# Kernel tuning notes

Measured on AMD Instinct MI355X. Metric: run time of the kernel, lower is better.

The kernel has to match this reference:

```python
import jax, jax.numpy as jnp
import numpy as np
from jax import lax


def setup_inputs() -> dict:
    key = jax.random.key(0)
    ks = jax.random.split(key, 4)
    B, Cin, H, W = 8, 64, 128, 128
    Cout, kh, kw = 64, 3, 3
    K = kh * kw
    x = jax.random.normal(ks[0], (B, Cin, H, W), jnp.float32)
    # small init so predicted offsets stay in a sensible range
    w_offset = jax.random.normal(ks[1], (2 * K, Cin, kh, kw), jnp.float32) * 0.01
    b_offset = jnp.zeros((2 * K,), jnp.float32)
    w_conv = jax.random.normal(ks[2], (Cout, Cin, kh, kw), jnp.float32) * (1.0 / np.sqrt(Cin * K))
    b_conv = jax.random.normal(ks[3], (Cout,), jnp.float32) * 0.01
    return dict(x=x, w_offset=w_offset, b_offset=b_offset, w_conv=w_conv, b_conv=b_conv)


def _deform_conv2d(x, offset, w, b, stride=(1, 1), padding=(1, 1), dilation=(1, 1)):
    B, Cin, Hin, Win = x.shape
    Cout, _, kh, kw = w.shape
    K = kh * kw
    sh, sw = stride; ph, pw = padding; dh, dw = dilation
    Hout = (Hin + 2 * ph - dh * (kh - 1) - 1) // sh + 1
    Wout = (Win + 2 * pw - dw * (kw - 1) - 1) // sw + 1
    # torchvision layout: [B, K, (dy,dx), Hout, Wout]
    off = offset.reshape(B, K, 2, Hout, Wout)
    dy, dx = off[:, :, 0], off[:, :, 1]
    hs = jnp.arange(Hout, dtype=x.dtype) * sh - ph          # [Hout]
    ws = jnp.arange(Wout, dtype=x.dtype) * sw - pw          # [Wout]
    ky = jnp.repeat(jnp.arange(kh, dtype=x.dtype) * dh, kw)  # [K]
    kx = jnp.tile(jnp.arange(kw, dtype=x.dtype) * dw, kh)    # [K]
    py = dy + (ky[:, None, None] + hs[None, :, None])[None]  # [B,K,Hout,Wout]
    px = dx + (kx[:, None, None] + ws[None, None, :])[None]

    def sample(img, py, px):
        y0 = jnp.floor(py); x0 = jnp.floor(px)
        wy1 = py - y0; wx1 = px - x0
        wy0 = 1.0 - wy1; wx0 = 1.0 - wx1

        def gather(yy, xx, wgt):
            valid = (yy >= 0) & (yy <= Hin - 1) & (xx >= 0) & (xx <= Win - 1)
            yi = jnp.clip(yy, 0, Hin - 1).astype(jnp.int32)
            xi = jnp.clip(xx, 0, Win - 1).astype(jnp.int32)
            vals = img[:, yi, xi]  # [Cin,K,Hout,Wout]
            return vals * (wgt * valid)[None]

        return (gather(y0, x0, wy0 * wx0) + gather(y0, x0 + 1, wy0 * wx1)
                + gather(y0 + 1, x0, wy1 * wx0) + gather(y0 + 1, x0 + 1, wy1 * wx1))

    sampled = jax.vmap(sample)(x, py, px)  # [B,Cin,K,Hout,Wout]
    out = jnp.einsum('bckhw,ock->bohw', sampled, w.reshape(Cout, Cin, K))
    return out + b[None, :, None, None]


def reference(x, w_offset, b_offset, w_conv, b_conv):
    # offset-predicting conv (stride 1, same padding, dilation 1)
    offset = lax.conv_general_dilated(
        x, w_offset, window_strides=(1, 1), padding=[(1, 1), (1, 1)],
        rhs_dilation=(1, 1), dimension_numbers=('NCHW', 'OIHW', 'NCHW'))
    offset = offset + b_offset[None, :, None, None]
    # deformable conv v1 (mask is None in _get_deformation)
    return _deform_conv2d(x, offset, w_conv, b_conv)
```

## Files before the change

### kernel.cpp

```cpp
#include <hip/hip_runtime.h>
#include <stdint.h>

#define H 128
#define W 128
#define CIN 64
#define COUT 64
#define NB 8
#define WR 4
#define WC 16
#define CW 20
#define NR 8
#define PLANE 162
#define REDS 260

typedef __attribute__((ext_vector_type(4))) float f32x4;
typedef __attribute__((ext_vector_type(2))) _Float16 f16x2;
typedef __attribute__((ext_vector_type(8))) _Float16 f16x8;
typedef __attribute__((ext_vector_type(4))) unsigned int u32x4;
typedef __attribute__((ext_vector_type(2))) unsigned int u32x2;

__device__ __forceinline__ f16x2 bch2(unsigned u) { return __builtin_bit_cast(f16x2, u); }
__device__ __forceinline__ unsigned bcu(f16x2 v) { return __builtin_bit_cast(unsigned, v); }

__global__ __launch_bounds__(256) void x_to_nhwc(const float* __restrict__ x,
                                                 _Float16* __restrict__ xt) {
    __shared__ _Float16 tile[W][68];
    int bh = blockIdx.x;
    int h = bh & (H - 1), b = bh >> 7;
    int t = threadIdx.x;
    #pragma unroll
    for (int i = 0; i < 8; ++i) {
        int idx = i * 256 + t;
        int c = idx >> 5;
        int w4 = (idx & 31) << 2;
        f32x4 v = *(const f32x4*)(x + (((size_t)(b * CIN + c) * H + h) * W + w4));
        #pragma unroll
        for (int j = 0; j < 4; ++j) tile[w4 + j][c] = (_Float16)v[j];
    }
    __syncthreads();
    _Float16* dst = xt + (size_t)bh * W * CIN;
    #pragma unroll
    for (int i = 0; i < 8; ++i) {
        int idx = i * 256 + t;
        int w = idx >> 4;
        int c4 = (idx & 15) << 2;
        *(uint2*)(dst + (size_t)w * CIN + c4) = *(const uint2*)&tile[w][c4];
    }
}

__global__ __launch_bounds__(256) void prep_w(const float* __restrict__ wo,
                                              const float* __restrict__ wc,
                                              _Float16* __restrict__ wao2,
                                              _Float16* __restrict__ wac2) {
    int t = blockIdx.x * 256 + threadIdx.x;
    if (t < 18432) {
        int j = t & 7, l = (t >> 3) & 63, m = (t >> 9) & 1, kk = t >> 10;
        int cout = m * 16 + (l & 15);
        int cin = (kk & 1) * 32 + ((l >> 4) << 3) + j;
        wao2[t] = (cout < 18) ? (_Float16)wo[(cout * 64 + cin) * 9 + (kk >> 1)]
                              : (_Float16)0.f;
    } else if (t < 18432 + 36864) {
        int u = t - 18432;
        int j = u & 7, l = (u >> 3) & 63, m = (u >> 9) & 3, kk = u >> 11;
        int cout = m * 16 + (l & 15);
        int cin = (kk & 1) * 32 + ((l >> 4) << 3) + j;
        wac2[u] = (_Float16)wc[(cout * 64 + cin) * 9 + (kk >> 1)];
    }
}

__global__ __launch_bounds__(256, 4) void deform_fused(const _Float16* __restrict__ xt,
                                                       const _Float16* __restrict__ wao2,
                                                       const _Float16* __restrict__ wac2,
                                                       const float* __restrict__ bo,
                                                       const float* __restrict__ bconv,
                                                       float* __restrict__ out) {
    __shared__ u32x4 s_x[8 * PLANE];
    __shared__ float s_meta[4][432];

    int bid = blockIdx.x;
    int b = bid & 7;
    int r = bid >> 3;
    int h0 = ((r >> 3) & 31) << 2;
    int w0 = (r & 7) << 4;
    int vy = h0 - 2, vx = w0 - 2;

    int t = threadIdx.x;
    int lane = t & 63, wv = t >> 6;
    int q = wv & 1;
    int half = wv >> 1;
    int pcol = lane & 15, hq = lane >> 4;
    int pl = half * 4 + hq;
    int r0 = h0 + 2 * q, r1 = r0 + 1;
    int wp = w0 + pcol;

    const _Float16* xb = xt + (size_t)b * H * W * CIN;

    for (int i = t; i < NR * CW * 8; i += 256) {
        int ch = i & 7;
        int q2 = i >> 3;
        int rr = q2 / CW;
        int cs = q2 - rr * CW;
        int row = min(max(vy + rr, 0), H - 1);
        int col = min(max(vx + cs, 0), W - 1);
        s_x[ch * PLANE + rr * CW + cs] =
            *(const u32x4*)(xb + (size_t)(row * W + col) * CIN + (ch << 3));
    }
    __syncthreads();

    const u32x4* sp = s_x + pl * PLANE;

    f32x4 aA0 = {}, aA1 = {}, aB0 = {}, aB1 = {};
    #pragma unroll
    for (int k = 0; k < 9; ++k) {
        int ky = k / 3 - 1, kx = k % 3 - 1;
        int xx = wp + kx;
        bool vx_ok = (unsigned)xx < (unsigned)W;
        int xc = min(max(xx, 0), W - 1) - vx;
        int yyA = r0 + ky, yyB = r1 + ky;
        int sA = (min(max(yyA, 0), H - 1) - vy) * CW + xc;
        int sB = (min(max(yyB, 0), H - 1) - vy) * CW + xc;
        u32x4 vA = sp[sA], vB = sp[sB];
        u32x4 z = {};
        if (!(vx_ok && (unsigned)yyA < (unsigned)H)) vA = z;
        if (!(vx_ok && (unsigned)yyB < (unsigned)H)) vB = z;
        f16x8 bfA = __builtin_bit_cast(f16x8, vA);
        f16x8 bfB = __builtin_bit_cast(f16x8, vB);
        const _Float16* wb = wao2 + (size_t)(4 * k + 2 * half) * 512 + lane * 8;
        f16x8 a0 = *(const f16x8*)(wb);
        f16x8 a1 = *(const f16x8*)(wb + 512);
        aA0 = __builtin_amdgcn_mfma_f32_16x16x32_f16(a0, bfA, aA0, 0, 0, 0);
        aA1 = __builtin_amdgcn_mfma_f32_16x16x32_f16(a1, bfA, aA1, 0, 0, 0);
        aB0 = __builtin_amdgcn_mfma_f32_16x16x32_f16(a0, bfB, aB0, 0, 0, 0);
        aB1 = __builtin_amdgcn_mfma_f32_16x16x32_f16(a1, bfB, aB1, 0, 0, 0);
    }

    if (half == 1) {
        float* scA = s_meta[2 * q] + lane * 6;
        scA[0] = aA0[0]; scA[1] = aA0[1]; scA[2] = aA0[2]; scA[3] = aA0[3];
        scA[4] = aA1[0]; scA[5] = aA1[1];
        float* scB = s_meta[2 * q + 1] + lane * 6;
        scB[0] = aB0[0]; scB[1] = aB0[1]; scB[2] = aB0[2]; scB[3] = aB0[3];
        scB[4] = aB1[0]; scB[5] = aB1[1];
    }
    __syncthreads();

    if (half == 0) {
        const float* scA = s_meta[2 * q] + lane * 6;
        const float* scB = s_meta[2 * q + 1] + lane * 6;
        float pA[6], pB[6];
        #pragma unroll
        for (int i = 0; i < 6; ++i) { pA[i] = scA[i]; pB[i] = scB[i]; }
        aA0[0] += pA[0]; aA0[1] += pA[1]; aA0[2] += pA[2]; aA0[3] += pA[3];
        aA1[0] += pA[4]; aA1[1] += pA[5];
        aB0[0] += pB[0]; aB0[1] += pB[1]; aB0[2] += pB[2]; aB0[3] += pB[3];
        aB1[0] += pB[4]; aB1[1] += pB[5];

        auto setup = [&](float* mrow, int row, int k, float dy, float dx) {
            float py = (float)(row + k / 3 - 1) + dy;
            float px = (float)(wp + k % 3 - 1) + dx;
            float y0f = floorf(py), x0f = floorf(px);
            float fy = py - y0f, fx = px - x0f;
            float vy0 = (y0f >= 0.f  && y0f <= 127.f) ? 1.f : 0.f;
            float vy1 = (y0f >= -1.f && y0f <= 126.f) ? 1.f : 0.f;
            float vx0 = (x0f >= 0.f  && x0f <= 127.f) ? 1.f : 0.f;
            float vx1 = (x0f >= -1.f && x0f <= 126.f) ? 1.f : 0.f;
            float g0 = (1.f - fy) * (1.f - fx) * vy0 * vx0;
            float g1 = (1.f - fy) * fx         * vy0 * vx1;
            float g2 = fy * (1.f - fx)         * vy1 * vx0;
            float g3 = fy * fx                 * vy1 * vx1;
            int y0i = (int)fminf(fmaxf(y0f, 0.f), 127.f);
            int x0i = (int)fminf(fmaxf(x0f, 0.f), 127.f);
            int y1i = (int)fminf(fmaxf(y0f + 1.f, 0.f), 127.f);
            int x1i = (int)fminf(fmaxf(x0f + 1.f, 0.f), 127.f);
            unsigned dxb = (unsigned)(x1i - x0i);
            unsigned dyb = (unsigned)(y1i - y0i);
            bool inw = (y0i >= vy) && (y1i <= vy + NR - 1) &&
                       (x0i >= vx) && (x1i <= vx + CW - 1);
            unsigned s00 = inw ? (unsigned)((y0i - vy) * CW + (x0i - vx)) : 0u;
            unsigned a00 = (unsigned)(y0i * W + x0i);
            unsigned awv = s00 | (dxb << 9) | (dyb << 10) | (inw ? 0u : (1u << 11)) | (a00 << 12);
            int idx = k * 16 + pcol;
            ((unsigned*)mrow)[idx] = awv;
            ((unsigned*)mrow)[144 + 2 * idx]     = bcu((f16x2){(_Float16)g0, (_Float16)g1});
            ((unsigned*)mrow)[144 + 2 * idx + 1] = bcu((f16x2){(_Float16)g2, (_Float16)g3});
        };
        f32x4 bo4 = *(const f32x4*)(bo + 4 * hq);
        setup(s_meta[2 * q],     r0, 2 * hq,     aA0[0] + bo4[0], aA0[1] + bo4[1]);
        setup(s_meta[2 * q],     r0, 2 * hq + 1, aA0[2] + bo4[2], aA0[3] + bo4[3]);
        setup(s_meta[2 * q + 1], r1, 2 * hq,     aB0[0] + bo4[0], aB0[1] + bo4[1]);
        setup(s_meta[2 * q + 1], r1, 2 * hq + 1, aB0[2] + bo4[2], aB0[3] + bo4[3]);
        if (hq == 0) {
            setup(s_meta[2 * q],     r0, 8, aA1[0] + bo[16], aA1[1] + bo[17]);
            setup(s_meta[2 * q + 1], r1, 8, aB1[0] + bo[16], aB1[1] + bo[17]);
        }
    }
    __syncthreads();

    const _Float16* xh = xb + (pl << 3);
    const unsigned* mA = (const unsigned*)s_meta[2 * q];
    const unsigned* mB = (const unsigned*)s_meta[2 * q + 1];
    f32x4 accA[4] = {}, accB[4] = {};

    #pragma unroll
    for (int k = 0; k < 9; ++k) {
        int idx = k * 16 + pcol;
        unsigned awA = mA[idx];
        unsigned awB = mB[idx];
        u32x2 wqA = *(const u32x2*)&mA[144 + 2 * idx];
        u32x2 wqB = *(const u32x2*)&mB[144 + 2 * idx];
        unsigned sA = awA & 511u, dxA = (awA >> 9) & 1u, dyA = (awA >> 10) & 1u;
        unsigned sB = awB & 511u, dxB = (awB >> 9) & 1u, dyB = (awB >> 10) & 1u;
        u32x4 a00 = sp[sA], a01 = sp[sA + dxA];
        u32x4 a10 = sp[sA + dyA * CW], a11 = sp[sA + dyA * CW + dxA];
        u32x4 b00 = sp[sB], b01 = sp[sB + dxB];
        u32x4 b10 = sp[sB + dyB * CW], b11 = sp[sB + dyB * CW + dxB];
        if (__builtin_expect((awA & (1u << 11)) != 0u, 0)) {
            unsigned a0_ = awA >> 12;
            a00 = *(const u32x4*)(xh + (size_t)a0_ * CIN);
            a01 = *(const u32x4*)(xh + (size_t)(a0_ + dxA) * CIN);
            a10 = *(const u32x4*)(xh + (size_t)(a0_ + (dyA << 7)) * CIN);
            a11 = *(const u32x4*)(xh + (size_t)(a0_ + (dyA << 7) + dxA) * CIN);
        }
        if (__builtin_expect((awB & (1u << 11)) != 0u, 0)) {
            unsigned b0_ = awB >> 12;
            b00 = *(const u32x4*)(xh + (size_t)b0_ * CIN);
            b01 = *(const u32x4*)(xh + (size_t)(b0_ + dxB) * CIN);
            b10 = *(const u32x4*)(xh + (size_t)(b0_ + (dyB << 7)) * CIN);
            b11 = *(const u32x4*)(xh + (size_t)(b0_ + (dyB << 7) + dxB) * CIN);
        }
        f16x2 wa = bch2(wqA[0]), wc_ = bch2(wqA[1]);
        f16x2 A00 = (f16x2){wa[0], wa[0]},  A01 = (f16x2){wa[1], wa[1]};
        f16x2 A10 = (f16x2){wc_[0], wc_[0]}, A11 = (f16x2){wc_[1], wc_[1]};
        f16x2 wb_ = bch2(wqB[0]), wd_ = bch2(wqB[1]);
        f16x2 B00 = (f16x2){wb_[0], wb_[0]}, B01 = (f16x2){wb_[1], wb_[1]};
        f16x2 B10 = (f16x2){wd_[0], wd_[0]}, B11 = (f16x2){wd_[1], wd_[1]};
        u32x4 frA, frB;
        #pragma unroll
        for (int d = 0; d < 4; ++d) {
            f16x2 vA = bch2(a00[d]) * A00 + bch2(a01[d]) * A01
                     + bch2(a10[d]) * A10 + bch2(a11[d]) * A11;
            f16x2 vB = bch2(b00[d]) * B00 + bch2(b01[d]) * B01
                     + bch2(b10[d]) * B10 + bch2(b11[d]) * B11;
            frA[d] = bcu(vA);
            frB[d] = bcu(vB);
        }
        f16x8 bfA = __builtin_bit_cast(f16x8, frA);
        f16x8 bfB = __builtin_bit_cast(f16x8, frB);
        const _Float16* ab = wac2 + (size_t)(8 * k + 4 * half) * 512 + lane * 8;
        #pragma unroll
        for (int m = 0; m < 4; ++m) {
            f16x8 wm = *(const f16x8*)(ab + m * 512);
            accA[m] = __builtin_amdgcn_mfma_f32_16x16x32_f16(wm, bfA, accA[m], 0, 0, 0);
            accB[m] = __builtin_amdgcn_mfma_f32_16x16x32_f16(wm, bfB, accB[m], 0, 0, 0);
        }
    }

    __syncthreads();
    float* red = (float*)s_x;
    if (half == 0) {
        #pragma unroll
        for (int m = 0; m < 4; ++m)
            #pragma unroll
            for (int r2 = 0; r2 < 4; ++r2)
                red[(m * 4 + r2) * REDS + q * 64 + lane] = accA[m][r2];
    }
    __syncthreads();
    if (half == 1) {
        #pragma unroll
        for (int m = 0; m < 4; ++m) {
            f32x4 bc4 = *(const f32x4*)(bconv + m * 16 + (hq << 2));
            #pragma unroll
            for (int r2 = 0; r2 < 4; ++r2) {
                int co = (m << 4) + (hq << 2) + r2;
                float v = accA[m][r2] + red[(m * 4 + r2) * REDS + q * 64 + lane] + bc4[r2];
                out[(((size_t)b * COUT + co) * H + r0) * W + wp] = v;
            }
        }
    }
    __syncthreads();
    if (half == 0) {
        #pragma unroll
        for (int m = 0; m < 4; ++m)
            #pragma unroll
            for (int r2 = 0; r2 < 4; ++r2)
                red[(m * 4 + r2) * REDS + q * 64 + lane] = accB[m][r2];
    }
    __syncthreads();
    if (half == 1) {
        #pragma unroll
        for (int m = 0; m < 4; ++m) {
            f32x4 bc4 = *(const f32x4*)(bconv + m * 16 + (hq << 2));
            #pragma unroll
            for (int r2 = 0; r2 < 4; ++r2) {
                int co = (m << 4) + (hq << 2) + r2;
                float v = accB[m][r2] + red[(m * 4 + r2) * REDS + q * 64 + lane] + bc4[r2];
                out[(((size_t)b * COUT + co) * H + r1) * W + wp] = v;
            }
        }
    }
}

extern "C" void kernel_launch(void* const* d_in, const int* in_sizes, int n_in,
                              void* d_out, int out_size, void* d_ws, size_t ws_size,
                              hipStream_t stream) {
    const float* x  = (const float*)d_in[0];
    const float* wo = (const float*)d_in[1];
    const float* bo = (const float*)d_in[2];
    const float* wc = (const float*)d_in[3];
    const float* bc = (const float*)d_in[4];
    float* out = (float*)d_out;

    _Float16* xt   = (_Float16*)d_ws;
    _Float16* wao2 = (_Float16*)((char*)d_ws + (size_t)NB * H * W * CIN * 2);
    _Float16* wac2 = wao2 + 18432;

    x_to_nhwc<<<NB * H, 256, 0, stream>>>(x, xt);
    prep_w<<<(18432 + 36864 + 255) / 256, 256, 0, stream>>>(wo, wc, wao2, wac2);
    deform_fused<<<NB * H * W / (WR * WC), 256, 0, stream>>>(xt, wao2, wac2, bo, bc, out);
}
```

Measured before the change: 49.89 us.

## Enlarge fused deform-conv tile to 8x16 pixels, four rows per wave

```diff
diff --git a/kernel.cpp b/kernel.cpp
--- a/kernel.cpp
+++ b/kernel.cpp
@@ -6,12 +6,11 @@
 #define CIN 64
 #define COUT 64
 #define NB 8
-#define WR 4
+#define WR 8
 #define WC 16
 #define CW 20
-#define NR 8
-#define PLANE 162
-#define REDS 260
+#define NR 12
+#define PLANE 242
 
 typedef __attribute__((ext_vector_type(4))) float f32x4;
 typedef __attribute__((ext_vector_type(2))) _Float16 f16x2;
@@ -68,19 +67,20 @@
     }
 }
 
-__global__ __launch_bounds__(256, 4) void deform_fused(const _Float16* __restrict__ xt,
+__global__ __launch_bounds__(256, 3) void deform_fused(const _Float16* __restrict__ xt,
                                                        const _Float16* __restrict__ wao2,
                                                        const _Float16* __restrict__ wac2,
                                                        const float* __restrict__ bo,
                                                        const float* __restrict__ bconv,
                                                        float* __restrict__ out) {
-    __shared__ u32x4 s_x[8 * PLANE];
-    __shared__ float s_meta[4][432];
+    __shared__ __align__(16) char smem[44800];
+    u32x4* s_x   = (u32x4*)smem;
+    float* s_metaF = (float*)(smem + 30976);
 
     int bid = blockIdx.x;
     int b = bid & 7;
     int r = bid >> 3;
-    int h0 = ((r >> 3) & 31) << 2;
+    int h0 = ((r >> 3) & 15) << 3;
     int w0 = (r & 7) << 4;
     int vy = h0 - 2, vx = w0 - 2;
 
@@ -90,7 +90,7 @@
     int half = wv >> 1;
     int pcol = lane & 15, hq = lane >> 4;
     int pl = half * 4 + hq;
-    int r0 = h0 + 2 * q, r1 = r0 + 1;
+    int rbase = h0 + 4 * q;
     int wp = w0 + pcol;
 
     const _Float16* xb = xt + (size_t)b * H * W * CIN;
@@ -109,52 +109,47 @@
 
     const u32x4* sp = s_x + pl * PLANE;
 
-    f32x4 aA0 = {}, aA1 = {}, aB0 = {}, aB1 = {};
+    f32x4 aO0[4] = {}, aO1[4] = {};
     #pragma unroll
     for (int k = 0; k < 9; ++k) {
         int ky = k / 3 - 1, kx = k % 3 - 1;
         int xx = wp + kx;
         bool vx_ok = (unsigned)xx < (unsigned)W;
         int xc = min(max(xx, 0), W - 1) - vx;
-        int yyA = r0 + ky, yyB = r1 + ky;
-        int sA = (min(max(yyA, 0), H - 1) - vy) * CW + xc;
-        int sB = (min(max(yyB, 0), H - 1) - vy) * CW + xc;
-        u32x4 vA = sp[sA], vB = sp[sB];
-        u32x4 z = {};
-        if (!(vx_ok && (unsigned)yyA < (unsigned)H)) vA = z;
-        if (!(vx_ok && (unsigned)yyB < (unsigned)H)) vB = z;
-        f16x8 bfA = __builtin_bit_cast(f16x8, vA);
-        f16x8 bfB = __builtin_bit_cast(f16x8, vB);
         const _Float16* wb = wao2 + (size_t)(4 * k + 2 * half) * 512 + lane * 8;
         f16x8 a0 = *(const f16x8*)(wb);
         f16x8 a1 = *(const f16x8*)(wb + 512);
-        aA0 = __builtin_amdgcn_mfma_f32_16x16x32_f16(a0, bfA, aA0, 0, 0, 0);
-        aA1 = __builtin_amdgcn_mfma_f32_16x16x32_f16(a1, bfA, aA1, 0, 0, 0);
-        aB0 = __builtin_amdgcn_mfma_f32_16x16x32_f16(a0, bfB, aB0, 0, 0, 0);
-        aB1 = __builtin_amdgcn_mfma_f32_16x16x32_f16(a1, bfB, aB1, 0, 0, 0);
+        #pragma unroll
+        for (int rr = 0; rr < 4; ++rr) {
+            int yy = rbase + rr + ky;
+            int s = (min(max(yy, 0), H - 1) - vy) * CW + xc;
+            u32x4 v = sp[s];
+            u32x4 z = {};
+            if (!(vx_ok && (unsigned)yy < (unsigned)H)) v = z;
+            f16x8 bf = __builtin_bit_cast(f16x8, v);
+            aO0[rr] = __builtin_amdgcn_mfma_f32_16x16x32_f16(a0, bf, aO0[rr], 0, 0, 0);
+            aO1[rr] = __builtin_amdgcn_mfma_f32_16x16x32_f16(a1, bf, aO1[rr], 0, 0, 0);
+        }
     }
 
     if (half == 1) {
-        float* scA = s_meta[2 * q] + lane * 6;
-        scA[0] = aA0[0]; scA[1] = aA0[1]; scA[2] = aA0[2]; scA[3] = aA0[3];
-        scA[4] = aA1[0]; scA[5] = aA1[1];
-        float* scB = s_meta[2 * q + 1] + lane * 6;
-        scB[0] = aB0[0]; scB[1] = aB0[1]; scB[2] = aB0[2]; scB[3] = aB0[3];
-        scB[4] = aB1[0]; scB[5] = aB1[1];
+        #pragma unroll
+        for (int rr = 0; rr < 4; ++rr) {
+            float* sc = s_metaF + (4 * q + rr) * 432 + lane * 6;
+            sc[0] = aO0[rr][0]; sc[1] = aO0[rr][1]; sc[2] = aO0[rr][2]; sc[3] = aO0[rr][3];
+            sc[4] = aO1[rr][0]; sc[5] = aO1[rr][1];
+        }
     }
     __syncthreads();
 
     if (half == 0) {
-        const float* scA = s_meta[2 * q] + lane * 6;
-        const float* scB = s_meta[2 * q + 1] + lane * 6;
-        float pA[6], pB[6];
-        #pragma unroll
-        for (int i = 0; i < 6; ++i) { pA[i] = scA[i]; pB[i] = scB[i]; }
-        aA0[0] += pA[0]; aA0[1] += pA[1]; aA0[2] += pA[2]; aA0[3] += pA[3];
-        aA1[0] += pA[4]; aA1[1] += pA[5];
-        aB0[0] += pB[0]; aB0[1] += pB[1]; aB0[2] += pB[2]; aB0[3] += pB[3];
-        aB1[0] += pB[4]; aB1[1] += pB[5];
-
+        #pragma unroll
+        for (int rr = 0; rr < 4; ++rr) {
+            const float* sc = s_metaF + (4 * q + rr) * 432 + lane * 6;
+            aO0[rr][0] += sc[0]; aO0[rr][1] += sc[1];
+            aO0[rr][2] += sc[2]; aO0[rr][3] += sc[3];
+            aO1[rr][0] += sc[4]; aO1[rr][1] += sc[5];
+        }
         auto setup = [&](float* mrow, int row, int k, float dy, float dx) {
             float py = (float)(row + k / 3 - 1) + dy;
             float px = (float)(wp + k % 3 - 1) + dx;
@@ -185,116 +180,87 @@
             ((unsigned*)mrow)[144 + 2 * idx + 1] = bcu((f16x2){(_Float16)g2, (_Float16)g3});
         };
         f32x4 bo4 = *(const f32x4*)(bo + 4 * hq);
-        setup(s_meta[2 * q],     r0, 2 * hq,     aA0[0] + bo4[0], aA0[1] + bo4[1]);
-        setup(s_meta[2 * q],     r0, 2 * hq + 1, aA0[2] + bo4[2], aA0[3] + bo4[3]);
-        setup(s_meta[2 * q + 1], r1, 2 * hq,     aB0[0] + bo4[0], aB0[1] + bo4[1]);
-        setup(s_meta[2 * q + 1], r1, 2 * hq + 1, aB0[2] + bo4[2], aB0[3] + bo4[3]);
-        if (hq == 0) {
-            setup(s_meta[2 * q],     r0, 8, aA1[0] + bo[16], aA1[1] + bo[17]);
-            setup(s_meta[2 * q + 1], r1, 8, aB1[0] + bo[16], aB1[1] + bo[17]);
+        #pragma unroll
+        for (int rr = 0; rr < 4; ++rr) {
+            float* mrow = s_metaF + (4 * q + rr) * 432;
+            int row = rbase + rr;
+            setup(mrow, row, 2 * hq,     aO0[rr][0] + bo4[0], aO0[rr][1] + bo4[1]);
+            setup(mrow, row, 2 * hq + 1, aO0[rr][2] + bo4[2], aO0[rr][3] + bo4[3]);
+            if (hq == 0) setup(mrow, row, 8, aO1[rr][0] + bo[16], aO1[rr][1] + bo[17]);
         }
     }
     __syncthreads();
 
     const _Float16* xh = xb + (pl << 3);
-    const unsigned* mA = (const unsigned*)s_meta[2 * q];
-    const unsigned* mB = (const unsigned*)s_meta[2 * q + 1];
-    f32x4 accA[4] = {}, accB[4] = {};
+    f32x4 acc[4][4] = {};
 
     #pragma unroll
     for (int k = 0; k < 9; ++k) {
+        const _Float16* ab = wac2 + (size_t)(8 * k + 4 * half) * 512 + lane * 8;
+        f16x8 wm0 = *(const f16x8*)(ab);
+        f16x8 wm1 = *(const f16x8*)(ab + 512);
+        f16x8 wm2 = *(const f16x8*)(ab + 1024);
+        f16x8 wm3 = *(const f16x8*)(ab + 1536);
         int idx = k * 16 + pcol;
-        unsigned awA = mA[idx];
-        unsigned awB = mB[idx];
-        u32x2 wqA = *(const u32x2*)&mA[144 + 2 * idx];
-        u32x2 wqB = *(const u32x2*)&mB[144 + 2 * idx];
-        unsigned sA = awA & 511u, dxA = (awA >> 9) & 1u, dyA = (awA >> 10) & 1u;
-        unsigned sB = awB & 511u, dxB = (awB >> 9) & 1u, dyB = (awB >> 10) & 1u;
-        u32x4 a00 = sp[sA], a01 = sp[sA + dxA];
-        u32x4 a10 = sp[sA + dyA * CW], a11 = sp[sA + dyA * CW + dxA];
-        u32x4 b00 = sp[sB], b01 = sp[sB + dxB];
-        u32x4 b10 = sp[sB + dyB * CW], b11 = sp[sB + dyB * CW + dxB];
-        if (__builtin_expect((awA & (1u << 11)) != 0u, 0)) {
-            unsigned a0_ = awA >> 12;
-            a00 = *(const u32x4*)(xh + (size_t)a0_ * CIN);
-            a01 = *(const u32x4*)(xh + (size_t)(a0_ + dxA) * CIN);
-            a10 = *(const u32x4*)(xh + (size_t)(a0_ + (dyA << 7)) * CIN);
-            a11 = *(const u32x4*)(xh + (size_t)(a0_ + (dyA << 7) + dxA) * CIN);
-        }
-        if (__builtin_expect((awB & (1u << 11)) != 0u, 0)) {
-            unsigned b0_ = awB >> 12;
-            b00 = *(const u32x4*)(xh + (size_t)b0_ * CIN);
-            b01 = *(const u32x4*)(xh + (size_t)(b0_ + dxB) * CIN);
-            b10 = *(const u32x4*)(xh + (size_t)(b0_ + (dyB << 7)) * CIN);
-            b11 = *(const u32x4*)(xh + (size_t)(b0_ + (dyB << 7) + dxB) * CIN);
-        }
-        f16x2 wa = bch2(wqA[0]), wc_ = bch2(wqA[1]);
-        f16x2 A00 = (f16x2){wa[0], wa[0]},  A01 = (f16x2){wa[1], wa[1]};
-        f16x2 A10 = (f16x2){wc_[0], wc_[0]}, A11 = (f16x2){wc_[1], wc_[1]};
-        f16x2 wb_ = bch2(wqB[0]), wd_ = bch2(wqB[1]);
-        f16x2 B00 = (f16x2){wb_[0], wb_[0]}, B01 = (f16x2){wb_[1], wb_[1]};
-        f16x2 B10 = (f16x2){wd_[0], wd_[0]}, B11 = (f16x2){wd_[1], wd_[1]};
-        u32x4 frA, frB;
-        #pragma unroll
-        for (int d = 0; d < 4; ++d) {
-            f16x2 vA = bch2(a00[d]) * A00 + bch2(a01[d]) * A01
-                     + bch2(a10[d]) * A10 + bch2(a11[d]) * A11;
-            f16x2 vB = bch2(b00[d]) * B00 + bch2(b01[d]) * B01
-                     + bch2(b10[d]) * B10 + bch2(b11[d]) * B11;
-            frA[d] = bcu(vA);
-            frB[d] = bcu(vB);
-        }
-        f16x8 bfA = __builtin_bit_cast(f16x8, frA);
-        f16x8 bfB = __builtin_bit_cast(f16x8, frB);
-        const _Float16* ab = wac2 + (size_t)(8 * k + 4 * half) * 512 + lane * 8;
-        #pragma unroll
-        for (int m = 0; m < 4; ++m) {
-            f16x8 wm = *(const f16x8*)(ab + m * 512);
-            accA[m] = __builtin_amdgcn_mfma_f32_16x16x32_f16(wm, bfA, accA[m], 0, 0, 0);
-            accB[m] = __builtin_amdgcn_mfma_f32_16x16x32_f16(wm, bfB, accB[m], 0, 0, 0);
-        }
-    }
-
-    __syncthreads();
-    float* red = (float*)s_x;
+        #pragma unroll
+        for (int rr = 0; rr < 4; ++rr) {
+            const unsigned* mrow = (const unsigned*)(s_metaF + (4 * q + rr) * 432);
+            unsigned aw = mrow[idx];
+            u32x2 wq = *(const u32x2*)&mrow[144 + 2 * idx];
+            unsigned s0 = aw & 511u, dxb = (aw >> 9) & 1u, dyb = (aw >> 10) & 1u;
+            u32x4 c00 = sp[s0], c01 = sp[s0 + dxb];
+            u32x4 c10 = sp[s0 + dyb * CW], c11 = sp[s0 + dyb * CW + dxb];
+            if (__builtin_expect((aw & (1u << 11)) != 0u, 0)) {
+                unsigned a0_ = aw >> 12;
+                c00 = *(const u32x4*)(xh + (size_t)a0_ * CIN);
+                c01 = *(const u32x4*)(xh + (size_t)(a0_ + dxb) * CIN);
+                c10 = *(const u32x4*)(xh + (size_t)(a0_ + (dyb << 7)) * CIN);
+                c11 = *(const u32x4*)(xh + (size_t)(a0_ + (dyb << 7) + dxb) * CIN);
+            }
+            f16x2 wab = bch2(wq[0]), wcd = bch2(wq[1]);
+            f16x2 w00d = (f16x2){wab[0], wab[0]}, w01d = (f16x2){wab[1], wab[1]};
+            f16x2 w10d = (f16x2){wcd[0], wcd[0]}, w11d = (f16x2){wcd[1], wcd[1]};
+            u32x4 fr;
+            #pragma unroll
+            for (int d = 0; d < 4; ++d) {
+                f16x2 v = bch2(c00[d]) * w00d + bch2(c01[d]) * w01d
+                        + bch2(c10[d]) * w10d + bch2(c11[d]) * w11d;
+                fr[d] = bcu(v);
+            }
+            f16x8 bf = __builtin_bit_cast(f16x8, fr);
+            acc[rr][0] = __builtin_amdgcn_mfma_f32_16x16x32_f16(wm0, bf, acc[rr][0], 0, 0, 0);
+            acc[rr][1] = __builtin_amdgcn_mfma_f32_16x16x32_f16(wm1, bf, acc[rr][1], 0, 0, 0);
+            acc[rr][2] = __builtin_amdgcn_mfma_f32_16x16x32_f16(wm2, bf, acc[rr][2], 0, 0, 0);
+            acc[rr][3] = __builtin_amdgcn_mfma_f32_16x16x32_f16(wm3, bf, acc[rr][3], 0, 0, 0);
+        }
+    }
+
+    __syncthreads();
+    float* red = (float*)smem;
     if (half == 0) {
         #pragma unroll
-        for (int m = 0; m < 4; ++m)
+        for (int rr = 0; rr < 4; ++rr)
             #pragma unroll
-            for (int r2 = 0; r2 < 4; ++r2)
-                red[(m * 4 + r2) * REDS + q * 64 + lane] = accA[m][r2];
+            for (int m = 0; m < 4; ++m)
+                #pragma unroll
+                for (int r2 = 0; r2 < 4; ++r2)
+                    red[((m * 4 + r2) * 8 + q * 4 + rr) * 64 + lane] = acc[rr][m][r2];
     }
     __syncthreads();
     if (half == 1) {
         #pragma unroll
-        for (int m = 0; m < 4; ++m) {
-            f32x4 bc4 = *(const f32x4*)(bconv + m * 16 + (hq << 2));
+        for (int rr = 0; rr < 4; ++rr) {
+            int row = rbase + rr;
             #pragma unroll
-            for (int r2 = 0; r2 < 4; ++r2) {
-                int co = (m << 4) + (hq << 2) + r2;
-                float v = accA[m][r2] + red[(m * 4 + r2) * REDS + q * 64 + lane] + bc4[r2];
-                out[(((size_t)b * COUT + co) * H + r0) * W + wp] = v;
-            }
-        }
-    }
-    __syncthreads();
-    if (half == 0) {
-        #pragma unroll
-        for (int m = 0; m < 4; ++m)
-            #pragma unroll
-            for (int r2 = 0; r2 < 4; ++r2)
-                red[(m * 4 + r2) * REDS + q * 64 + lane] = accB[m][r2];
-    }
-    __syncthreads();
-    if (half == 1) {
-        #pragma unroll
-        for (int m = 0; m < 4; ++m) {
-            f32x4 bc4 = *(const f32x4*)(bconv + m * 16 + (hq << 2));
-            #pragma unroll
-            for (int r2 = 0; r2 < 4; ++r2) {
-                int co = (m << 4) + (hq << 2) + r2;
-                float v = accB[m][r2] + red[(m * 4 + r2) * REDS + q * 64 + lane] + bc4[r2];
-                out[(((size_t)b * COUT + co) * H + r1) * W + wp] = v;
+            for (int m = 0; m < 4; ++m) {
+                f32x4 bc4 = *(const f32x4*)(bconv + m * 16 + (hq << 2));
+                #pragma unroll
+                for (int r2 = 0; r2 < 4; ++r2) {
+                    int co = (m << 4) + (hq << 2) + r2;
+                    float v = acc[rr][m][r2]
+                            + red[((m * 4 + r2) * 8 + q * 4 + rr) * 64 + lane] + bc4[r2];
+                    out[(((size_t)b * COUT + co) * H + row) * W + wp] = v;
+                }
             }
         }
     }
```

Measured after the change: 55.30 us. +10.8%, slower.
